# Kernel tuning notes

Hardware: AMD Instinct MI355X
Metric: run time of the kernel (lower is better)

Reference implementation:

```python
import jax, jax.numpy as jnp
import numpy as np

ENC, PRED, JOINT_H, VOCAB, BLANK, MAXSYM = 1024, 320, 512, 29, 28, 6


def _lstm_step(x, h, c, Wi, Wh, b):
    # torch LSTM gate order: i, f, g, o
    gates = x @ Wi.T + h @ Wh.T + b
    i, f, g, o = jnp.split(gates, 4, axis=-1)
    c2 = jax.nn.sigmoid(f) * c + jax.nn.sigmoid(i) * jnp.tanh(g)
    h2 = jax.nn.sigmoid(o) * jnp.tanh(c2)
    return h2, c2


def setup_inputs() -> dict:
    key = jax.random.key(0)
    ks = jax.random.split(key, 13)
    B, T = 32, 48
    s = 0.1
    return {
        "x": jax.random.normal(ks[0], (B, T, ENC), jnp.float32),
        "out_lens": jax.random.randint(ks[1], (B,), T // 2, T + 1),
        "emb": s * jax.random.normal(ks[2], (VOCAB - 1, PRED), jnp.float32),
        "Wi0": s * jax.random.normal(ks[3], (4 * PRED, PRED), jnp.float32),
        "Wh0": s * jax.random.normal(ks[4], (4 * PRED, PRED), jnp.float32),
        "b0": s * jax.random.normal(ks[5], (4 * PRED,), jnp.float32),
        "Wi1": s * jax.random.normal(ks[6], (4 * PRED, PRED), jnp.float32),
        "Wh1": s * jax.random.normal(ks[7], (4 * PRED, PRED), jnp.float32),
        "b1": s * jax.random.normal(ks[8], (4 * PRED,), jnp.float32),
        "Wj1": s * jax.random.normal(ks[9], (JOINT_H, ENC + PRED), jnp.float32),
        "bj1": s * jax.random.normal(ks[10], (JOINT_H,), jnp.float32),
        "Wj2": s * jax.random.normal(ks[11], (VOCAB, JOINT_H), jnp.float32),
        "bj2": s * jax.random.normal(ks[12], (VOCAB,), jnp.float32),
    }


def reference(x, out_lens, emb, Wi0, Wh0, b0, Wi1, Wh1, b1, Wj1, bj1, Wj2, bj2):
    B, T, _ = x.shape
    rows = jnp.arange(B)
    n_steps = T * MAXSYM  # upper bound on greedy-loop iterations

    def pred_step(label, h, c):
        # SOS (-1) -> zero embedding, matching model.prediction(None, ...)
        e = jnp.where((label >= 0)[:, None], emb[jnp.clip(label, 0)], 0.0)
        h0, c0 = _lstm_step(e, h[0], c[0], Wi0, Wh0, b0)
        h1, c1 = _lstm_step(h0, h[1], c[1], Wi1, Wh1, b1)
        return h1, jnp.stack([h0, h1]), jnp.stack([c0, c1])

    def joint(f, g):
        z = jnp.concatenate([f, g], axis=-1)  # [B, ENC+PRED]
        return jax.nn.relu(z @ Wj1.T + bj1) @ Wj2.T + bj2  # [B, VOCAB]

    def body(state, _):
        h, c, lt, lc, f, ti, sa = state
        last = lt[rows, lc]                      # last emitted symbol (or -1 = SOS)
        g, h_p, c_p = pred_step(last, h, c)
        logits = joint(f, g)
        k = jnp.argmax(logits, axis=-1).astype(jnp.int32)
        blankness = k == BLANK
        ti = ti + blankness.astype(jnp.int32)
        blank_vec = ti >= out_lens               # finished sequences
        sa = sa * (~blankness)                   # reset symbol count on blank
        not_blank = ~(blank_vec | blankness)
        # masked hidden-state scatter: hidden[:, idx, :] = hidden_prime[:, idx, :]
        h = jnp.where(not_blank[None, :, None], h_p, h)
        c = jnp.where(not_blank[None, :, None], c_p, c)
        lc = lc + not_blank.astype(jnp.int32)
        # index_put_ accumulate of (k - SOS) into label tensor initialized to SOS=-1
        lt = lt.at[rows, lc].add(jnp.where(not_blank, k + 1, 0))
        sa = sa + not_blank.astype(jnp.int32)
        need_add = sa >= MAXSYM                  # force time advance at max symbols
        ti = ti + need_add.astype(jnp.int32)
        sa = sa * (sa < MAXSYM)
        # data-dependent re-fetch of encoder frame (clamped like time_idxs.min(max_lens))
        f = x[rows, jnp.minimum(ti, T - 1)]
        return (h, c, lt, lc, f, ti, sa), None

    h0 = jnp.zeros((2, B, PRED), x.dtype)
    c0 = jnp.zeros((2, B, PRED), x.dtype)
    lt0 = jnp.full((B, n_steps), -1, jnp.int32)
    lc0 = jnp.zeros((B,), jnp.int32)
    ti0 = jnp.zeros((B,), jnp.int32)
    sa0 = jnp.zeros((B,), jnp.int32)
    f0 = x[:, 0, :]
    state, _ = jax.lax.scan(body, (h0, c0, lt0, lc0, f0, ti0, sa0), None, length=n_steps)
    _, _, lt, lc, _, _, _ = state
    # labels for item i are lt[i, 1:lc[i]+1]; return padded tensor + lengths
    return lt, lc
```

## Files before the change

kernel.cpp:

```cpp
#include <hip/hip_runtime.h>
#include <math.h>

#define B_ 32
#define T_ 48
#define ENC_ 1024
#define PRED_ 320
#define JH_ 512
#define NJ_ 1344
#define VOCAB_ 29
#define BLANK_ 28
#define MAXSYM_ 6
#define NSTEPS_ 288
#define BDEC 512
#define GRID_DEC 160
#define NG 8
#define GBAT 4
#define NBLK 20
#define JPB 16
#define NJB 16
#define VPB 32
#define HPAD 324

#define FPRE_OFF 0
#define WE_OFF   786432
#define H0C2_OFF 822272
#define H1C2_OFF 842752
#define PL2_OFF  863232
#define INT_OFF  928768
#define NTAGS    2560
#define STAMPF   106496

__device__ __forceinline__ float sigm(float v) { return 1.0f / (1.0f + expf(-v)); }

__device__ __forceinline__ int  ld_i(const int* p)   { return __hip_atomic_load((int*)p, __ATOMIC_RELAXED, __HIP_MEMORY_SCOPE_AGENT); }
__device__ __forceinline__ void st_i(int* p, int v)  { __hip_atomic_store(p, v, __ATOMIC_RELAXED, __HIP_MEMORY_SCOPE_AGENT); }

__device__ __forceinline__ void st_pair(float* p, float v, int stamp) {
    float2 x; x.x = v; x.y = __int_as_float(stamp);
    asm volatile("global_store_dwordx2 %0, %1, off sc0 sc1" :: "v"(p), "v"(x) : "memory");
}
__device__ __forceinline__ void ldc4_2(const float* p0, const float* p1,
                                       float4& r0, float4& r1) {
    asm volatile("global_load_dwordx4 %0, %2, off sc0 sc1\n\t"
                 "global_load_dwordx4 %1, %3, off sc0 sc1\n\t"
                 "s_waitcnt vmcnt(0)"
                 : "=&v"(r0), "=&v"(r1)
                 : "v"(p0), "v"(p1)
                 : "memory");
}

#define PIDX(g, ks, jl, gb) ((((g)*8 + (ks))*16 + (jl))*4 + (gb))

__global__ void k_init(float* __restrict__ ws, int* __restrict__ out) {
    int idx = blockIdx.x * blockDim.x + threadIdx.x;
    int stride = gridDim.x * blockDim.x;
    for (int i = idx; i < STAMPF; i += stride) ws[H0C2_OFF + i] = 0.0f;
    int* wi = (int*)ws;
    for (int i = idx; i < NTAGS; i += stride) wi[INT_OFF + i] = 0;
    for (int i = idx; i < B_*NSTEPS_; i += stride) out[i] = -1;
    if (idx < B_) out[B_*NSTEPS_ + idx] = 0;
}

__global__ __launch_bounds__(256) void k_we(const float* __restrict__ emb,
                                            const float* __restrict__ Wi0,
                                            float* __restrict__ ws) {
    __shared__ float es[PRED_];
    int l = blockIdx.x / 5;
    int rq = blockIdx.x % 5;
    int t = threadIdx.x;
    if (t < PRED_) es[t] = emb[l*PRED_ + t];
    if (t + 256 < PRED_) es[t + 256] = emb[l*PRED_ + t + 256];
    __syncthreads();
    int r = rq*256 + t;
    const float4* wr = (const float4*)(Wi0 + (size_t)r*PRED_);
    float acc = 0.0f;
    #pragma unroll 4
    for (int k4 = 0; k4 < PRED_/4; ++k4) {
        float4 w = wr[k4];
        acc += w.x*es[4*k4] + w.y*es[4*k4+1] + w.z*es[4*k4+2] + w.w*es[4*k4+3];
    }
    ws[WE_OFF + l*(4*PRED_) + r] = acc;
}

__global__ __launch_bounds__(256) void k_fpre(const float* __restrict__ x,
                                              const float* __restrict__ Wj1,
                                              const float* __restrict__ bj1,
                                              float* __restrict__ ws) {
    __shared__ float As[B_][129];
    __shared__ float Bs[64][129];
    int tt = blockIdx.x >> 3;
    int jb = blockIdx.x & 7;
    int tid = threadIdx.x;
    int b = tid >> 3, jq = tid & 7;
    float acc[8] = {0,0,0,0,0,0,0,0};
    for (int kc = 0; kc < ENC_; kc += 128) {
        for (int i = tid; i < B_*128; i += 256) {
            int bb = i >> 7, kk = i & 127;
            As[bb][kk] = x[((size_t)bb*T_ + tt)*ENC_ + kc + kk];
        }
        for (int i = tid; i < 64*128; i += 256) {
            int jj = i >> 7, kk = i & 127;
            Bs[jj][kk] = Wj1[((size_t)(jb*64 + jj))*NJ_ + kc + kk];
        }
        __syncthreads();
        for (int kk = 0; kk < 128; ++kk) {
            float a = As[b][kk];
            #pragma unroll
            for (int u = 0; u < 8; ++u) acc[u] += a * Bs[jq*8 + u][kk];
        }
        __syncthreads();
    }
    #pragma unroll
    for (int u = 0; u < 8; ++u) {
        int j = jb*64 + jq*8 + u;
        ws[FPRE_OFF + ((size_t)b*T_ + tt)*JH_ + j] = acc[u] + bj1[j];
    }
}

__global__ __launch_bounds__(BDEC) void k_decode(
    const int* __restrict__ out_lens,
    const float* __restrict__ Wh0, const float* __restrict__ b0,
    const float* __restrict__ Wi1, const float* __restrict__ Wh1,
    const float* __restrict__ b1,
    const float* __restrict__ Wj1,
    const float* __restrict__ Wj2, const float* __restrict__ bj2,
    float* __restrict__ ws, int* __restrict__ out)
{
    const int tid = threadIdx.x;
    const int grp = blockIdx.x & 7;
    const int lb  = blockIdx.x >> 3;
    const int j0  = lb * JPB;
    const int v0  = lb * VPB;
    const int bb0 = grp * GBAT;

    float* H0C2g = ws + H0C2_OFF + grp*2560;
    float* H1C2g = ws + H1C2_OFF + grp*2560;
    float* PL2g  = ws + PL2_OFF  + grp*8192;
    const float* WE = ws + WE_OFF;
    const float* FP = ws + FPRE_OFF;
    int* wi = (int*)ws;
    int* tagD = wi + INT_OFF + grp*320;

    __shared__ __align__(16) float wi1_s[64*HPAD];
    __shared__ __align__(16) float hs0[GBAT*HPAD];
    __shared__ __align__(16) float hs1[GBAT*HPAD];
    __shared__ float parts[2048];
    __shared__ float parts2[2048];
    __shared__ float P0a[256], P0b[256], P1s[256];
    __shared__ float c0cur[64], c0cand[64], c1cur[64], c1cand[64];
    __shared__ float we_s[28][64];
    __shared__ float b0_s[64], b1_s[64], bj2_s[32];
    __shared__ float wj2t[VPB*33];
    __shared__ float jg_c[VPB*GBAT];
    __shared__ float hid_s[GBAT*33];
    __shared__ float logits_s[GBAT*33];
    __shared__ int ti_l[GBAT], last_l[GBAT], sa_l[GBAT], lc_l[GBAT], olen_s[GBAT];
    __shared__ unsigned s_masks[2];

    for (int i = tid; i < 64*PRED_; i += BDEC) {
        int r = i / PRED_, c = i % PRED_;
        int g = r >> 4, jj = r & 15;
        wi1_s[r*HPAD + c] = Wi1[((size_t)(g*PRED_ + j0 + jj))*PRED_ + c];
    }
    if (lb < NJB) {
        for (int i = tid; i < VPB*32; i += BDEC) {
            int v = i >> 5, l = i & 31;
            wj2t[v*33 + l] = (l < VOCAB_) ? Wj2[(size_t)l*JH_ + v0 + v] : 0.f;
        }
    }
    for (int i = tid; i < 28*64; i += BDEC) {
        int ls = i >> 6, r = i & 63;
        int g = r >> 4, jj = r & 15;
        we_s[ls][r] = WE[(size_t)ls*(4*PRED_) + g*PRED_ + j0 + jj];
    }
    if (tid < 64) {
        int g = tid >> 4, jj = tid & 15;
        b0_s[tid] = b0[g*PRED_ + j0 + jj];
        b1_s[tid] = b1[g*PRED_ + j0 + jj];
        c0cur[tid]=0.f; c0cand[tid]=0.f; c1cur[tid]=0.f; c1cand[tid]=0.f;
    }
    if (tid < VOCAB_) bj2_s[tid] = bj2[tid];
    if (tid < GBAT) {
        olen_s[tid] = out_lens[bb0 + tid];
        ti_l[tid] = 0; last_l[tid] = -1; sa_l[tid] = 0; lc_l[tid] = 0;
    }
    for (int i = tid; i < GBAT*HPAD; i += BDEC) { hs0[i] = 0.f; hs1[i] = 0.f; }
    if (tid < 256) P0a[tid] = 0.f;
    __syncthreads();

    const int gb  = tid & 3;
    const int jl  = (tid >> 2) & 15;
    const int ks  = tid >> 6;
    unsigned nbm = 0xfu, actm = 0xfu;

    for (int s = 0; s < NSTEPS_; ++s) {
        const int par = s & 1;
        const int st = s + 1;

        float f_reg = 0.f;
        if (lb < NJB && tid < 128) {
            int v_ = tid & 31, g2_ = tid >> 5;
            if ((actm >> g2_) & 1) {
                int tm = min(ti_l[g2_], T_ - 1);
                f_reg = FP[((size_t)(bb0+g2_)*T_ + tm)*JH_ + v0 + v_];
            }
        }

        if (nbm) {
            if (tid < 64) {
                int g2 = tid & 3, jj = tid >> 2;
                if ((nbm >> g2) & 1) {
                    int ls = last_l[g2];
                    float gt[4];
                    #pragma unroll
                    for (int g = 0; g < 4; ++g) {
                        int r = g*16 + jj;
                        float v = P0a[r*4 + g2] + b0_s[r];
                        if (ls >= 0) v += we_s[ls][r];
                        gt[g] = v;
                    }
                    float cn = sigm(gt[1])*c0cur[tid] + sigm(gt[0])*tanhf(gt[2]);
                    float hn = sigm(gt[3])*tanhf(cn);
                    c0cand[tid] = cn;
                    hs0[g2*HPAD + j0 + jj] = hn;
                    st_pair(&H0C2g[(lb*64 + tid)*2], hn, st);
                }
            }
            {
                const float* hr = &hs1[gb*HPAD];
                int k0 = ks * 40;
                float a0=0.f,a1=0.f,a2=0.f,a3=0.f;
                const float* w0 = Wh1 + ((size_t)(0*PRED_ + j0 + jl))*PRED_;
                const float* w1 = Wh1 + ((size_t)(1*PRED_ + j0 + jl))*PRED_;
                const float* w2 = Wh1 + ((size_t)(2*PRED_ + j0 + jl))*PRED_;
                const float* w3 = Wh1 + ((size_t)(3*PRED_ + j0 + jl))*PRED_;
                #pragma unroll 10
                for (int kk = k0; kk < k0 + 40; kk += 4) {
                    float4 h = *(const float4*)&hr[kk];
                    float4 q0 = *(const float4*)(w0 + kk);
                    float4 q1 = *(const float4*)(w1 + kk);
                    float4 q2 = *(const float4*)(w2 + kk);
                    float4 q3 = *(const float4*)(w3 + kk);
                    a0 += q0.x*h.x+q0.y*h.y+q0.z*h.z+q0.w*h.w;
                    a1 += q1.x*h.x+q1.y*h.y+q1.z*h.z+q1.w*h.w;
                    a2 += q2.x*h.x+q2.y*h.y+q2.z*h.z+q2.w*h.w;
                    a3 += q3.x*h.x+q3.y*h.y+q3.z*h.z+q3.w*h.w;
                }
                parts[PIDX(0,ks,jl,gb)] = a0;
                parts[PIDX(1,ks,jl,gb)] = a1;
                parts[PIDX(2,ks,jl,gb)] = a2;
                parts[PIDX(3,ks,jl,gb)] = a3;
            }
            __syncthreads();
            if (tid < 256) {
                int r = tid >> 2, g2 = tid & 3;
                int g = r >> 4, jj = r & 15;
                float v = 0.f;
                #pragma unroll
                for (int k = 0; k < 8; ++k) v += parts[PIDX(g,k,jj,g2)];
                P1s[r*4 + g2] = v;
            }
            {
                int b = tid >> 4, jj = tid & 15;
                if (tid < 320 && b != lb) {
                    const bool n0=(nbm>>0)&1, n1=(nbm>>1)&1, n2=(nbm>>2)&1, n3=(nbm>>3)&1;
                    const float* a0 = H0C2g + tid*8;
                    const float* a1 = a0 + 4;
                    float4 r0, r1;
                    for (;;) {
                        ldc4_2(a0, a1, r0, r1);
                        bool ok = (!n0 || __float_as_int(r0.y)==st)
                               && (!n1 || __float_as_int(r0.w)==st)
                               && (!n2 || __float_as_int(r1.y)==st)
                               && (!n3 || __float_as_int(r1.w)==st);
                        if (ok) break;
                        __builtin_amdgcn_s_sleep(1);
                    }
                    if (n0) hs0[0*HPAD + b*16 + jj] = r0.x;
                    if (n1) hs0[1*HPAD + b*16 + jj] = r0.z;
                    if (n2) hs0[2*HPAD + b*16 + jj] = r1.x;
                    if (n3) hs0[3*HPAD + b*16 + jj] = r1.z;
                }
            }
            __syncthreads();

            {
                const float* hr = &hs0[gb*HPAD];
                int k0 = ks * 40;
                float a0=0.f,a1=0.f,a2=0.f,a3=0.f;
                #pragma unroll 10
                for (int kk = k0; kk < k0 + 40; kk += 4) {
                    float4 h = *(const float4*)&hr[kk];
                    float4 q0 = *(const float4*)&wi1_s[(0*16+jl)*HPAD + kk];
                    float4 q1 = *(const float4*)&wi1_s[(1*16+jl)*HPAD + kk];
                    float4 q2 = *(const float4*)&wi1_s[(2*16+jl)*HPAD + kk];
                    float4 q3 = *(const float4*)&wi1_s[(3*16+jl)*HPAD + kk];
                    a0 += q0.x*h.x+q0.y*h.y+q0.z*h.z+q0.w*h.w;
                    a1 += q1.x*h.x+q1.y*h.y+q1.z*h.z+q1.w*h.w;
                    a2 += q2.x*h.x+q2.y*h.y+q2.z*h.z+q2.w*h.w;
                    a3 += q3.x*h.x+q3.y*h.y+q3.z*h.z+q3.w*h.w;
                }
                parts[PIDX(0,ks,jl,gb)] = a0;
                parts[PIDX(1,ks,jl,gb)] = a1;
                parts[PIDX(2,ks,jl,gb)] = a2;
                parts[PIDX(3,ks,jl,gb)] = a3;
            }
            __syncthreads();
            if (tid < 64) {
                int g2 = tid & 3, jj = tid >> 2;
                if ((nbm >> g2) & 1) {
                    float gt[4];
                    #pragma unroll
                    for (int g = 0; g < 4; ++g) {
                        int r = g*16 + jj;
                        float v = P1s[r*4 + g2] + b1_s[r];
                        #pragma unroll
                        for (int k = 0; k < 8; ++k) v += parts[PIDX(g,k,jj,g2)];
                        gt[g] = v;
                    }
                    float cn = sigm(gt[1])*c1cur[tid] + sigm(gt[0])*tanhf(gt[2]);
                    float hn = sigm(gt[3])*tanhf(cn);
                    c1cand[tid] = cn;
                    hs1[g2*HPAD + j0 + jj] = hn;
                    st_pair(&H1C2g[(lb*64 + tid)*2], hn, st);
                }
            }
            {
                const float* hr = &hs0[gb*HPAD];
                int k0 = ks * 40;
                float a0=0.f,a1=0.f;
                const float* w0 = Wh0 + ((size_t)(0*PRED_ + j0 + jl))*PRED_;
                const float* w1 = Wh0 + ((size_t)(1*PRED_ + j0 + jl))*PRED_;
                #pragma unroll 10
                for (int kk = k0; kk < k0 + 40; kk += 4) {
                    float4 h = *(const float4*)&hr[kk];
                    float4 q0 = *(const float4*)(w0 + kk);
                    float4 q1 = *(const float4*)(w1 + kk);
                    a0 += q0.x*h.x+q0.y*h.y+q0.z*h.z+q0.w*h.w;
                    a1 += q1.x*h.x+q1.y*h.y+q1.z*h.z+q1.w*h.w;
                }
                parts2[PIDX(0,ks,jl,gb)] = a0;
                parts2[PIDX(1,ks,jl,gb)] = a1;
            }
            {
                int b = tid >> 4, jj = tid & 15;
                if (tid < 320 && b != lb) {
                    const bool n0=(nbm>>0)&1, n1=(nbm>>1)&1, n2=(nbm>>2)&1, n3=(nbm>>3)&1;
                    const float* a0 = H1C2g + tid*8;
                    const float* a1 = a0 + 4;
                    float4 r0, r1;
                    for (;;) {
                        ldc4_2(a0, a1, r0, r1);
                        bool ok = (!n0 || __float_as_int(r0.y)==st)
                               && (!n1 || __float_as_int(r0.w)==st)
                               && (!n2 || __float_as_int(r1.y)==st)
                               && (!n3 || __float_as_int(r1.w)==st);
                        if (ok) break;
                        __builtin_amdgcn_s_sleep(1);
                    }
                    if (n0) hs1[0*HPAD + b*16 + jj] = r0.x;
                    if (n1) hs1[1*HPAD + b*16 + jj] = r0.z;
                    if (n2) hs1[2*HPAD + b*16 + jj] = r1.x;
                    if (n3) hs1[3*HPAD + b*16 + jj] = r1.z;
                }
            }
            __syncthreads();
        } else {
            if (lb < NJB) {
                if (tid < NBLK) { while (ld_i(&tagD[tid*16]) < s-1) __builtin_amdgcn_s_sleep(1); }
                __syncthreads();
            }
        }

        if (lb < NJB) {
            if (nbm) {
                int v = tid & 31, g2 = (tid >> 5) & 3, ks2 = tid >> 7;
                if ((nbm >> g2) & 1) {
                    const float* hr = &hs1[g2*HPAD];
                    const float* wt = Wj1 + ((size_t)(v0 + v))*NJ_ + ENC_ + ks2*80;
                    const float* hk = hr + ks2*80;
                    float p = 0.f;
                    #pragma unroll 20
                    for (int kk = 0; kk < 80; kk += 4) {
                        float4 w4 = *(const float4*)(wt + kk);
                        float4 h  = *(const float4*)(hk + kk);
                        p += w4.x*h.x + w4.y*h.y + w4.z*h.z + w4.w*h.w;
                    }
                    parts[(v*4 + g2)*4 + ks2] = p;
                }
            }
            __syncthreads();
            if (tid < 128) {
                int v = tid & 31, g2 = tid >> 5;
                if (nbm && ((nbm >> g2) & 1)) {
                    jg_c[v*4 + g2] = parts[(v*4+g2)*4+0] + parts[(v*4+g2)*4+1]
                                   + parts[(v*4+g2)*4+2] + parts[(v*4+g2)*4+3];
                }
                if ((actm >> g2) & 1) {
                    hid_s[g2*33 + v] = fmaxf(f_reg + jg_c[v*4 + g2], 0.f);
                }
            }
            __syncthreads();
            if (tid < 128) {
                int g2 = tid >> 5, l = tid & 31;
                const float* hb = &hid_s[g2*33];
                float acc = 0.f;
                #pragma unroll 8
                for (int v = 0; v < VPB; ++v) acc += wj2t[v*33 + l] * hb[v];
                st_pair(&PL2g[par*4096 + (lb*128 + tid)*2], acc, st);
            }
        }

        if (nbm) {
            {
                const float* hr = &hs0[gb*HPAD];
                int k0 = ks * 40;
                float a2=0.f,a3=0.f;
                const float* w2 = Wh0 + ((size_t)(2*PRED_ + j0 + jl))*PRED_;
                const float* w3 = Wh0 + ((size_t)(3*PRED_ + j0 + jl))*PRED_;
                #pragma unroll 10
                for (int kk = k0; kk < k0 + 40; kk += 4) {
                    float4 h = *(const float4*)&hr[kk];
                    float4 q2 = *(const float4*)(w2 + kk);
                    float4 q3 = *(const float4*)(w3 + kk);
                    a2 += q2.x*h.x+q2.y*h.y+q2.z*h.z+q2.w*h.w;
                    a3 += q3.x*h.x+q3.y*h.y+q3.z*h.z+q3.w*h.w;
                }
                parts2[PIDX(2,ks,jl,gb)] = a2;
                parts2[PIDX(3,ks,jl,gb)] = a3;
            }
            __syncthreads();
            if (tid < 256) {
                int r = tid >> 2, g2 = tid & 3;
                int g = r >> 4, jj = r & 15;
                float v = 0.f;
                #pragma unroll
                for (int k = 0; k < 8; ++k) v += parts2[PIDX(g,k,jj,g2)];
                P0b[r*4 + g2] = v;
            }
        }

        {
            int p0 = tid * 4;
            const float* a0 = PL2g + par*4096 + p0*2;
            float4 r0, r1;
            for (;;) {
                ldc4_2(a0, a0 + 4, r0, r1);
                if (__float_as_int(r0.y)==st && __float_as_int(r0.w)==st &&
                    __float_as_int(r1.y)==st && __float_as_int(r1.w)==st) break;
                __builtin_amdgcn_s_sleep(1);
            }
            parts[p0+0]=r0.x; parts[p0+1]=r0.z; parts[p0+2]=r1.x; parts[p0+3]=r1.z;
        }
        __syncthreads();
        if (tid < 128) {
            float v = 0.f;
            #pragma unroll
            for (int jb = 0; jb < 16; ++jb) v += parts[jb*128 + tid];
            int g2 = tid >> 5, l = tid & 31;
            logits_s[g2*33 + l] = (l < VOCAB_) ? (v + bj2_s[l]) : -1e30f;
        }
        __syncthreads();

        if (tid < 64) {
            bool nbb = false, actb = false;
            if (tid < GBAT && ((actm >> tid) & 1)) {
                const int g2 = tid;
                float best = -1e30f; int bi = 0;
                for (int l = 0; l < VOCAB_; ++l) {
                    float v = logits_s[g2*33 + l];
                    if (v > best) { best = v; bi = l; }
                }
                const int blankness = (bi == BLANK_) ? 1 : 0;
                int tiv = ti_l[g2] + blankness;
                if (tiv >= olen_s[g2]) {
                    ti_l[g2] = tiv;
                } else {
                    int notb = 1 - blankness;
                    int sav = blankness ? 0 : sa_l[g2];
                    int nl = last_l[g2];
                    int lcn = lc_l[g2];
                    if (notb) {
                        lcn += 1;
                        if (lb == g2) {
                            int bglob = bb0 + g2;
                            if (lcn < NSTEPS_) st_i(&out[bglob*NSTEPS_ + lcn], bi);
                            st_i(&out[B_*NSTEPS_ + bglob], lcn);
                        }
                        nl = bi;
                        sav += 1;
                    }
                    if (sav >= MAXSYM_) { tiv += 1; sav = 0; }
                    ti_l[g2] = tiv; sa_l[g2] = sav; last_l[g2] = nl; lc_l[g2] = lcn;
                    nbb = (notb != 0); actb = true;
                }
            }
            unsigned long long bn = __ballot(nbb);
            unsigned long long ba = __ballot(actb);
            if (tid == 0) { s_masks[0] = (unsigned)bn; s_masks[1] = (unsigned)ba; }
        }
        __syncthreads();
        const unsigned nbm_new = s_masks[0];
        actm = s_masks[1];
        if (tid < 64) {
            if ((nbm_new >> (tid & 3)) & 1) { c0cur[tid] = c0cand[tid]; c1cur[tid] = c1cand[tid]; }
        }
        if (tid < 256) {
            if ((nbm_new >> (tid & 3)) & 1) P0a[tid] = P0b[tid];
        }
        __syncthreads();
        nbm = nbm_new;
        if (tid == 0) st_i(&tagD[lb*16], s + 1);
        if (!actm) break;
    }
}

extern "C" void kernel_launch(void* const* d_in, const int* in_sizes, int n_in,
                              void* d_out, int out_size, void* d_ws, size_t ws_size,
                              hipStream_t stream) {
    const float* x    = (const float*)d_in[0];
    const int*   olen = (const int*)d_in[1];
    const float* emb  = (const float*)d_in[2];
    const float* Wi0  = (const float*)d_in[3];
    const float* Wh0  = (const float*)d_in[4];
    const float* b0   = (const float*)d_in[5];
    const float* Wi1  = (const float*)d_in[6];
    const float* Wh1  = (const float*)d_in[7];
    const float* b1   = (const float*)d_in[8];
    const float* Wj1  = (const float*)d_in[9];
    const float* bj1  = (const float*)d_in[10];
    const float* Wj2  = (const float*)d_in[11];
    const float* bj2  = (const float*)d_in[12];
    float* ws = (float*)d_ws;
    int* out = (int*)d_out;

    hipLaunchKernelGGL(k_init, dim3(256), dim3(256), 0, stream, ws, out);
    hipLaunchKernelGGL(k_we,   dim3(28*5), dim3(256), 0, stream, emb, Wi0, ws);
    hipLaunchKernelGGL(k_fpre, dim3(T_*8), dim3(256), 0, stream, x, Wj1, bj1, ws);
    hipLaunchKernelGGL(k_decode, dim3(GRID_DEC), dim3(BDEC), 0, stream,
                       olen, Wh0, b0, Wi1, Wh1, b1, Wj1, Wj2, bj2, ws, out);
}
```

Before: 4.158 ms.

## Compute layer-0 LSTM redundantly per block instead of exchanging h0 slices

Each block now gathers the full Wh0·h partial-sum vector that peer blocks publish through stamped global slots, then computes all 320 layer-0 hidden units locally. This removes the separate spin-wait that exchanged layer-0 hidden slices between blocks in the middle of each step. The remaining wait moves to the start of the next step and depends on the previous non-blank step. In exchange, every block repeats the full layer-0 gate math, reads the embedding-gate term from global memory, and needs larger shared buffers.

```diff
diff --git a/kernel.cpp b/kernel.cpp
--- a/kernel.cpp
+++ b/kernel.cpp
@@ -23,12 +23,12 @@
 
 #define FPRE_OFF 0
 #define WE_OFF   786432
-#define H0C2_OFF 822272
-#define H1C2_OFF 842752
-#define PL2_OFF  863232
-#define INT_OFF  928768
+#define H1C2_OFF 822272
+#define PL2_OFF  842752
+#define P0C2_OFF 908288
+#define INT_OFF  990208
 #define NTAGS    2560
-#define STAMPF   106496
+#define STAMPF   167936
 
 __device__ __forceinline__ float sigm(float v) { return 1.0f / (1.0f + expf(-v)); }
 
@@ -48,13 +48,26 @@
                  : "v"(p0), "v"(p1)
                  : "memory");
 }
+__device__ __forceinline__ void ldc4_5(const float* p0, const float* p1, const float* p2,
+                                       const float* p3, const float* p4,
+                                       float4& r0, float4& r1, float4& r2, float4& r3, float4& r4) {
+    asm volatile("global_load_dwordx4 %0, %5, off sc0 sc1\n\t"
+                 "global_load_dwordx4 %1, %6, off sc0 sc1\n\t"
+                 "global_load_dwordx4 %2, %7, off sc0 sc1\n\t"
+                 "global_load_dwordx4 %3, %8, off sc0 sc1\n\t"
+                 "global_load_dwordx4 %4, %9, off sc0 sc1\n\t"
+                 "s_waitcnt vmcnt(0)"
+                 : "=&v"(r0), "=&v"(r1), "=&v"(r2), "=&v"(r3), "=&v"(r4)
+                 : "v"(p0), "v"(p1), "v"(p2), "v"(p3), "v"(p4)
+                 : "memory");
+}
 
 #define PIDX(g, ks, jl, gb) ((((g)*8 + (ks))*16 + (jl))*4 + (gb))
 
 __global__ void k_init(float* __restrict__ ws, int* __restrict__ out) {
     int idx = blockIdx.x * blockDim.x + threadIdx.x;
     int stride = gridDim.x * blockDim.x;
-    for (int i = idx; i < STAMPF; i += stride) ws[H0C2_OFF + i] = 0.0f;
+    for (int i = idx; i < STAMPF; i += stride) ws[H1C2_OFF + i] = 0.0f;
     int* wi = (int*)ws;
     for (int i = idx; i < NTAGS; i += stride) wi[INT_OFF + i] = 0;
     for (int i = idx; i < B_*NSTEPS_; i += stride) out[i] = -1;
@@ -133,9 +146,9 @@
     const int v0  = lb * VPB;
     const int bb0 = grp * GBAT;
 
-    float* H0C2g = ws + H0C2_OFF + grp*2560;
     float* H1C2g = ws + H1C2_OFF + grp*2560;
     float* PL2g  = ws + PL2_OFF  + grp*8192;
+    float* P0C2g = ws + P0C2_OFF + grp*10240;
     const float* WE = ws + WE_OFF;
     const float* FP = ws + FPRE_OFF;
     int* wi = (int*)ws;
@@ -146,10 +159,11 @@
     __shared__ __align__(16) float hs1[GBAT*HPAD];
     __shared__ float parts[2048];
     __shared__ float parts2[2048];
-    __shared__ float P0a[256], P0b[256], P1s[256];
-    __shared__ float c0cur[64], c0cand[64], c1cur[64], c1cand[64];
-    __shared__ float we_s[28][64];
-    __shared__ float b0_s[64], b1_s[64], bj2_s[32];
+    __shared__ float P0curf[5120];
+    __shared__ float c0curf[1280], c0candf[1280];
+    __shared__ float P1s[256];
+    __shared__ float c1cur[64], c1cand[64];
+    __shared__ float b0f_s[1280], b1_s[64], bj2_s[32];
     __shared__ float wj2t[VPB*33];
     __shared__ float jg_c[VPB*GBAT];
     __shared__ float hid_s[GBAT*33];
@@ -168,16 +182,15 @@
             wj2t[v*33 + l] = (l < VOCAB_) ? Wj2[(size_t)l*JH_ + v0 + v] : 0.f;
         }
     }
-    for (int i = tid; i < 28*64; i += BDEC) {
-        int ls = i >> 6, r = i & 63;
-        int g = r >> 4, jj = r & 15;
-        we_s[ls][r] = WE[(size_t)ls*(4*PRED_) + g*PRED_ + j0 + jj];
-    }
+    for (int i = tid; i < 1280; i += BDEC) {
+        b0f_s[i] = b0[i];
+        c0curf[i] = 0.f; c0candf[i] = 0.f;
+    }
+    for (int i = tid; i < 5120; i += BDEC) P0curf[i] = 0.f;
     if (tid < 64) {
         int g = tid >> 4, jj = tid & 15;
-        b0_s[tid] = b0[g*PRED_ + j0 + jj];
         b1_s[tid] = b1[g*PRED_ + j0 + jj];
-        c0cur[tid]=0.f; c0cand[tid]=0.f; c1cur[tid]=0.f; c1cand[tid]=0.f;
+        c1cur[tid] = 0.f; c1cand[tid] = 0.f;
     }
     if (tid < VOCAB_) bj2_s[tid] = bj2[tid];
     if (tid < GBAT) {
@@ -185,13 +198,13 @@
         ti_l[tid] = 0; last_l[tid] = -1; sa_l[tid] = 0; lc_l[tid] = 0;
     }
     for (int i = tid; i < GBAT*HPAD; i += BDEC) { hs0[i] = 0.f; hs1[i] = 0.f; }
-    if (tid < 256) P0a[tid] = 0.f;
     __syncthreads();
 
     const int gb  = tid & 3;
     const int jl  = (tid >> 2) & 15;
     const int ks  = tid >> 6;
     unsigned nbm = 0xfu, actm = 0xfu;
+    int last_nb = -1;
 
     for (int s = 0; s < NSTEPS_; ++s) {
         const int par = s & 1;
@@ -207,23 +220,51 @@
         }
 
         if (nbm) {
-            if (tid < 64) {
-                int g2 = tid & 3, jj = tid >> 2;
+            if (last_nb >= 0) {
+                const int pst = last_nb + 1;
+                int p0 = tid * 10;
+                const float* base = P0C2g + p0*2;
+                float4 q0, q1, q2, q3, q4;
+                for (;;) {
+                    ldc4_5(base, base+4, base+8, base+12, base+16, q0, q1, q2, q3, q4);
+                    bool ok = __float_as_int(q0.y)==pst && __float_as_int(q0.w)==pst
+                           && __float_as_int(q1.y)==pst && __float_as_int(q1.w)==pst
+                           && __float_as_int(q2.y)==pst && __float_as_int(q2.w)==pst
+                           && __float_as_int(q3.y)==pst && __float_as_int(q3.w)==pst
+                           && __float_as_int(q4.y)==pst && __float_as_int(q4.w)==pst;
+                    if (ok) break;
+                    __builtin_amdgcn_s_sleep(1);
+                }
+                float vv[10] = {q0.x,q0.z,q1.x,q1.z,q2.x,q2.z,q3.x,q3.z,q4.x,q4.z};
+                #pragma unroll
+                for (int i = 0; i < 10; ++i) {
+                    int p = p0 + i;
+                    int g2 = p & 3;
+                    if ((nbm >> g2) & 1) {
+                        int rl = (p >> 2) & 63, lbs = p >> 8;
+                        int r = (rl >> 4)*320 + lbs*16 + (rl & 15);
+                        P0curf[r*4 + g2] = vv[i];
+                    }
+                }
+            }
+            __syncthreads();
+
+            for (int idx = tid; idx < 1280; idx += BDEC) {
+                int g2 = idx & 3, j = idx >> 2;
                 if ((nbm >> g2) & 1) {
                     int ls = last_l[g2];
                     float gt[4];
                     #pragma unroll
                     for (int g = 0; g < 4; ++g) {
-                        int r = g*16 + jj;
-                        float v = P0a[r*4 + g2] + b0_s[r];
-                        if (ls >= 0) v += we_s[ls][r];
+                        int r = g*320 + j;
+                        float v = P0curf[r*4 + g2] + b0f_s[r];
+                        if (ls >= 0) v += WE[(size_t)ls*1280 + r];
                         gt[g] = v;
                     }
-                    float cn = sigm(gt[1])*c0cur[tid] + sigm(gt[0])*tanhf(gt[2]);
+                    float cn = sigm(gt[1])*c0curf[j*4 + g2] + sigm(gt[0])*tanhf(gt[2]);
                     float hn = sigm(gt[3])*tanhf(cn);
-                    c0cand[tid] = cn;
-                    hs0[g2*HPAD + j0 + jj] = hn;
-                    st_pair(&H0C2g[(lb*64 + tid)*2], hn, st);
+                    c0candf[j*4 + g2] = cn;
+                    hs0[g2*HPAD + j] = hn;
                 }
             }
             {
@@ -259,28 +300,6 @@
                 #pragma unroll
                 for (int k = 0; k < 8; ++k) v += parts[PIDX(g,k,jj,g2)];
                 P1s[r*4 + g2] = v;
-            }
-            {
-                int b = tid >> 4, jj = tid & 15;
-                if (tid < 320 && b != lb) {
-                    const bool n0=(nbm>>0)&1, n1=(nbm>>1)&1, n2=(nbm>>2)&1, n3=(nbm>>3)&1;
-                    const float* a0 = H0C2g + tid*8;
-                    const float* a1 = a0 + 4;
-                    float4 r0, r1;
-                    for (;;) {
-                        ldc4_2(a0, a1, r0, r1);
-                        bool ok = (!n0 || __float_as_int(r0.y)==st)
-                               && (!n1 || __float_as_int(r0.w)==st)
-                               && (!n2 || __float_as_int(r1.y)==st)
-                               && (!n3 || __float_as_int(r1.w)==st);
-                        if (ok) break;
-                        __builtin_amdgcn_s_sleep(1);
-                    }
-                    if (n0) hs0[0*HPAD + b*16 + jj] = r0.x;
-                    if (n1) hs0[1*HPAD + b*16 + jj] = r0.z;
-                    if (n2) hs0[2*HPAD + b*16 + jj] = r1.x;
-                    if (n3) hs0[3*HPAD + b*16 + jj] = r1.z;
-                }
             }
             __syncthreads();
 
@@ -436,7 +455,7 @@
                 float v = 0.f;
                 #pragma unroll
                 for (int k = 0; k < 8; ++k) v += parts2[PIDX(g,k,jj,g2)];
-                P0b[r*4 + g2] = v;
+                st_pair(&P0C2g[(lb*256 + tid)*2], v, st);
             }
         }
 
@@ -503,12 +522,13 @@
         const unsigned nbm_new = s_masks[0];
         actm = s_masks[1];
         if (tid < 64) {
-            if ((nbm_new >> (tid & 3)) & 1) { c0cur[tid] = c0cand[tid]; c1cur[tid] = c1cand[tid]; }
-        }
-        if (tid < 256) {
-            if ((nbm_new >> (tid & 3)) & 1) P0a[tid] = P0b[tid];
+            if ((nbm_new >> (tid & 3)) & 1) c1cur[tid] = c1cand[tid];
+        }
+        for (int i = tid; i < 1280; i += BDEC) {
+            if ((nbm_new >> (i & 3)) & 1) c0curf[i] = c0candf[i];
         }
         __syncthreads();
+        if (nbm) last_nb = s;
         nbm = nbm_new;
         if (tid == 0) st_i(&tagD[lb*16], s + 1);
         if (!actm) break;
```

New measurement: 5.406 ms. 1.3x slower.
